# Performance work log

Measured on AMD Instinct MI355X. Metric: run time of the kernel, lower is better.

## Reference

```python
import jax, jax.numpy as jnp
import numpy as np

B, S, HID = 1, 2048, 4096
H, HKV, D = 32, 8, 128
ROT = 64  # partial_rotary_factor = 0.5
EPS = 1e-6
SCALE = D ** -0.5


def setup_inputs() -> dict:
    key = jax.random.key(0)
    ks = jax.random.split(key, 8)
    return {
        "hidden_states": jax.random.normal(ks[0], (B, S, HID), jnp.float32),
        "cos": jax.random.uniform(ks[1], (B, S, ROT), jnp.float32),
        "sin": jax.random.uniform(ks[2], (B, S, ROT), jnp.float32),
        "Wq": jax.random.normal(ks[3], (H * D, HID), jnp.float32) * 0.02,
        "Wk": jax.random.normal(ks[4], (HKV * D, HID), jnp.float32) * 0.02,
        "Wv": jax.random.normal(ks[5], (HKV * D, HID), jnp.float32) * 0.02,
        "Wo": jax.random.normal(ks[6], (H * D, HID), jnp.float32).T * 0.02,  # [HID, H*D]
        "q_norm_w": jnp.ones((D,), jnp.float32),
        "k_norm_w": jnp.ones((D,), jnp.float32),
    }


def _rmsnorm(x, w):
    var = jnp.mean(jnp.square(x), axis=-1, keepdims=True)
    return x * jax.lax.rsqrt(var + EPS) * w


def _rotate_half(x):
    x1, x2 = jnp.split(x, 2, axis=-1)
    return jnp.concatenate([-x2, x1], axis=-1)


def reference(hidden_states, cos, sin, Wq, Wk, Wv, Wo, q_norm_w, k_norm_w):
    b, s, _ = hidden_states.shape
    q = (hidden_states @ Wq.T).reshape(b, s, H, D)
    k = (hidden_states @ Wk.T).reshape(b, s, HKV, D)
    v = (hidden_states @ Wv.T).reshape(b, s, HKV, D)
    # per-head QK RMSNorm
    q = _rmsnorm(q, q_norm_w)
    k = _rmsnorm(k, k_norm_w)
    # partial RoPE on first ROT dims; cos/sin broadcast over head dim (unsqueeze_dim=2)
    cs = cos[:, :, None, :]  # [B,S,1,ROT]
    sn = sin[:, :, None, :]
    q_rot, q_pass = q[..., :ROT], q[..., ROT:]
    k_rot, k_pass = k[..., :ROT], k[..., ROT:]
    q_rot = q_rot * cs + _rotate_half(q_rot) * sn
    k_rot = k_rot * cs + _rotate_half(k_rot) * sn
    q = jnp.concatenate([q_rot, q_pass], axis=-1)
    k = jnp.concatenate([k_rot, k_pass], axis=-1)
    # GQA: expand kv heads to query heads
    rep = H // HKV
    k = jnp.repeat(k, rep, axis=2)  # [B,S,H,D]
    v = jnp.repeat(v, rep, axis=2)
    # causal SDPA, bsnd layout
    scores = jnp.einsum("bqhd,bkhd->bhqk", q, k) * SCALE
    causal = jnp.tril(jnp.ones((s, s), bool))
    scores = jnp.where(causal, scores, jnp.finfo(scores.dtype).min)
    attn = jax.nn.softmax(scores, axis=-1)
    out = jnp.einsum("bhqk,bkhd->bqhd", attn, v).reshape(b, s, H * D)
    return out @ Wo.T
```

## Files before the change

kernel.cpp:

```cpp
#include <hip/hip_runtime.h>
#include <hip/hip_bf16.h>

typedef __attribute__((ext_vector_type(8))) short bf16x8;
typedef __attribute__((ext_vector_type(4))) float f32x4;
typedef __hip_bfloat16 bf16;

#define S_LEN 2048
#define HIDDEN 4096
#define NH 32
#define NKV 8
#define DH 128
#define ROTD 64
#define QKVW 6144
#define KOFF 4096
#define VOFF 5120
#define ATT_SCALE 0.08838834764831845f
#define RMS_EPS 1e-6f
#define KPITCH 136
#define VPITCH 72

static __device__ __forceinline__ unsigned short f2bu(float f) {
    bf16 h = __float2bfloat16(f);
    return __builtin_bit_cast(unsigned short, h);
}

static __device__ __forceinline__ void load_lds_16(const bf16* g, bf16* l) {
    __builtin_amdgcn_global_load_lds((const __attribute__((address_space(1))) void*)g,
                                     (__attribute__((address_space(3))) void*)l, 16, 0, 0);
}

__global__ __launch_bounds__(256) void cast_f32_bf16(const float* __restrict__ src,
                                                     unsigned short* __restrict__ dst, int n4) {
    int i = blockIdx.x * 256 + threadIdx.x;
    if (i >= n4) return;
    float4 v = reinterpret_cast<const float4*>(src)[i];
    ushort4 o;
    o.x = f2bu(v.x); o.y = f2bu(v.y); o.z = f2bu(v.z); o.w = f2bu(v.w);
    reinterpret_cast<ushort4*>(dst)[i] = o;
}

template <typename OutT>
__global__ __launch_bounds__(256) void gemm_lds(const bf16* __restrict__ A,
                                                const bf16* __restrict__ B,
                                                OutT* __restrict__ C,
                                                int M, int N, int K) {
    __shared__ bf16 As[128 * 32];
    __shared__ bf16 Bs[128 * 32];
    const int tid  = threadIdx.x;
    const int lane = tid & 63;
    const int wave = tid >> 6;
    const int lq   = lane & 15;
    const int quad = lane >> 4;
    const int m0 = blockIdx.y * 128;
    const int n0 = blockIdx.x * 128;
    const int wm = (wave & 1) * 64;
    const int wn = (wave >> 1) * 64;

    f32x4 acc[4][4] = {};

    const int ar = tid >> 2;
    const int ac = (tid & 3) * 8;
    const bf16* Ag0 = A + (size_t)(m0 + ar) * K + ac;
    const bf16* Ag1 = Ag0 + (size_t)64 * K;
    const bf16* Bg0 = B + (size_t)(n0 + ar) * K + ac;
    const bf16* Bg1 = Bg0 + (size_t)64 * K;
    bf16* Asl0 = As + wave * 512;
    bf16* Asl1 = As + wave * 512 + 2048;
    bf16* Bsl0 = Bs + wave * 512;
    bf16* Bsl1 = Bs + wave * 512 + 2048;

    for (int k0 = 0; k0 < K; k0 += 32) {
        load_lds_16(Ag0 + k0, Asl0);
        load_lds_16(Ag1 + k0, Asl1);
        load_lds_16(Bg0 + k0, Bsl0);
        load_lds_16(Bg1 + k0, Bsl1);
        __syncthreads();
        bf16x8 av[4], bv[4];
#pragma unroll
        for (int i = 0; i < 4; ++i)
            av[i] = *reinterpret_cast<const bf16x8*>(As + (wm + i * 16 + lq) * 32 + quad * 8);
#pragma unroll
        for (int i = 0; i < 4; ++i)
            bv[i] = *reinterpret_cast<const bf16x8*>(Bs + (wn + i * 16 + lq) * 32 + quad * 8);
#pragma unroll
        for (int mt = 0; mt < 4; ++mt)
#pragma unroll
            for (int nt = 0; nt < 4; ++nt)
                acc[mt][nt] = __builtin_amdgcn_mfma_f32_16x16x32_bf16(av[mt], bv[nt], acc[mt][nt], 0, 0, 0);
        __syncthreads();
    }

#pragma unroll
    for (int mt = 0; mt < 4; ++mt)
#pragma unroll
        for (int nt = 0; nt < 4; ++nt)
#pragma unroll
            for (int r = 0; r < 4; ++r) {
                float v = acc[mt][nt][r];
                size_t idx = (size_t)(m0 + wm + mt * 16 + quad * 4 + r) * N + n0 + wn + nt * 16 + lq;
                if constexpr (sizeof(OutT) == 2) C[idx] = __float2bfloat16(v);
                else                             C[idx] = v;
            }
}

__global__ __launch_bounds__(256) void norm_rope(bf16* __restrict__ buf,
                                                 const float* __restrict__ w,
                                                 const float* __restrict__ cosp,
                                                 const float* __restrict__ sinp,
                                                 int log2nh, int stride, int coloff) {
    const int lane = threadIdx.x & 63;
    const int wave = threadIdx.x >> 6;
    const int row  = blockIdx.x * 4 + wave;
    const int s    = row >> log2nh;
    const int hh   = row & ((1 << log2nh) - 1);
    bf16* p = buf + (size_t)s * stride + coloff + hh * DH;

    float x1 = __bfloat162float(p[lane]);
    float x2 = __bfloat162float(p[64 + lane]);

    float ss = x1 * x1 + x2 * x2;
#pragma unroll
    for (int off = 1; off < 64; off <<= 1) ss += __shfl_xor(ss, off);
    float rs = rsqrtf(ss * (1.0f / 128.0f) + RMS_EPS);

    float y1 = x1 * rs * w[lane];
    float y2 = x2 * rs * w[64 + lane];

    float partner = __shfl_xor(y1, 32);
    float c  = cosp[(size_t)s * ROTD + lane];
    float sn = sinp[(size_t)s * ROTD + lane];
    float rot = (lane < 32) ? (y1 * c - partner * sn) : (y1 * c + partner * sn);

    p[lane]      = __float2bfloat16(rot);
    p[64 + lane] = __float2bfloat16(y2);
}

__global__ __launch_bounds__(256) void transpose_v(const bf16* __restrict__ v,
                                                   bf16* __restrict__ vt,
                                                   int stride, int colofs) {
    __shared__ bf16 t[32][65];
    const int c0 = blockIdx.x * 32;
    const int s0 = blockIdx.y * 64;
    {
        const int j  = threadIdx.x & 31;
        const int i0 = threadIdx.x >> 5;
#pragma unroll
        for (int p = 0; p < 8; ++p) {
            int si = p * 8 + i0;
            t[j][si] = v[(size_t)(s0 + si) * stride + colofs + c0 + j];
        }
    }
    __syncthreads();
    {
        const int ii = threadIdx.x & 63;
        const int j0 = threadIdx.x >> 6;
#pragma unroll
        for (int p = 0; p < 8; ++p) {
            int c = p * 4 + j0;
            vt[(size_t)(c0 + c) * S_LEN + s0 + ii] = t[c][ii];
        }
    }
}

struct FlashSmem {
    bf16 Ks[64][KPITCH];
    bf16 Vs[128][VPITCH];
    bf16 Ps[4][16][VPITCH];
};

static __device__ __forceinline__ void attn_qblock(int q0, int n_iter, int h, int kvh,
                                                   const bf16* __restrict__ QKV,
                                                   const bf16* __restrict__ VT,
                                                   bf16* __restrict__ O,
                                                   FlashSmem* sm) {
    const int tid  = threadIdx.x;
    const int lane = tid & 63;
    const int wave = tid >> 6;
    const int lq   = lane & 15;
    const int quad = lane >> 4;
    const int qr0  = q0 + wave * 16;

    bf16x8 qf[4];
    const bf16* qrow = QKV + (size_t)(qr0 + lq) * QKVW + h * DH + quad * 8;
#pragma unroll
    for (int i = 0; i < 4; ++i) {
        bf16x8 qv = *reinterpret_cast<const bf16x8*>(qrow + 32 * i);
#pragma unroll
        for (int j = 0; j < 8; ++j) {
            bf16 b = __builtin_bit_cast(bf16, (unsigned short)qv[j]);
            qv[j] = (short)__builtin_bit_cast(unsigned short,
                        __float2bfloat16(__bfloat162float(b) * ATT_SCALE));
        }
        qf[i] = qv;
    }

    f32x4 o[8];
#pragma unroll
    for (int t2 = 0; t2 < 8; ++t2) o[t2] = (f32x4){0.f, 0.f, 0.f, 0.f};
    float m_i[4], l_i[4];
#pragma unroll
    for (int r = 0; r < 4; ++r) { m_i[r] = -1e30f; l_i[r] = 0.f; }

    const bf16* kg = QKV + (size_t)(tid >> 2) * QKVW + KOFF + kvh * DH + (tid & 3) * 32;
    const bf16* vg = VT + (size_t)(kvh * DH + (tid >> 1)) * S_LEN + (tid & 1) * 32;
    bf16* ksl = &sm->Ks[tid >> 2][(tid & 3) * 32];
    bf16* vsl = &sm->Vs[tid >> 1][(tid & 1) * 32];
    bf16* pb  = &sm->Ps[wave][0][0];

    bf16x8 kreg[4], vreg[4];
#pragma unroll
    for (int c = 0; c < 4; ++c) {
        kreg[c] = *reinterpret_cast<const bf16x8*>(kg + 8 * c);
        vreg[c] = *reinterpret_cast<const bf16x8*>(vg + 8 * c);
    }

    for (int kt = 0; kt < n_iter; ++kt) {
        const int k0 = kt * 64;
#pragma unroll
        for (int c = 0; c < 4; ++c) {
            *reinterpret_cast<bf16x8*>(ksl + 8 * c) = kreg[c];
            *reinterpret_cast<bf16x8*>(vsl + 8 * c) = vreg[c];
        }
        __syncthreads();
        if (kt + 1 < n_iter) {
            const size_t kadv = (size_t)(kt + 1) * 64;
#pragma unroll
            for (int c = 0; c < 4; ++c) {
                kreg[c] = *reinterpret_cast<const bf16x8*>(kg + kadv * QKVW + 8 * c);
                vreg[c] = *reinterpret_cast<const bf16x8*>(vg + kadv + 8 * c);
            }
        }

        float p[4][4];
#pragma unroll
        for (int t = 0; t < 4; ++t) {
            f32x4 sacc = (f32x4){0.f, 0.f, 0.f, 0.f};
#pragma unroll
            for (int i = 0; i < 4; ++i) {
                bf16x8 kf = *reinterpret_cast<const bf16x8*>(&sm->Ks[t * 16 + lq][quad * 8 + 32 * i]);
                sacc = __builtin_amdgcn_mfma_f32_16x16x32_bf16(qf[i], kf, sacc, 0, 0, 0);
            }
#pragma unroll
            for (int r = 0; r < 4; ++r) {
                int qi = qr0 + quad * 4 + r;
                int ki = k0 + t * 16 + lq;
                p[t][r] = (ki > qi) ? -1e30f : sacc[r];
            }
        }

        float rowmax[4];
#pragma unroll
        for (int r = 0; r < 4; ++r)
            rowmax[r] = fmaxf(fmaxf(p[0][r], p[1][r]), fmaxf(p[2][r], p[3][r]));
#pragma unroll
        for (int off = 1; off < 16; off <<= 1)
#pragma unroll
            for (int r = 0; r < 4; ++r) rowmax[r] = fmaxf(rowmax[r], __shfl_xor(rowmax[r], off));

        float alpha[4];
#pragma unroll
        for (int r = 0; r < 4; ++r) {
            float mn = fmaxf(m_i[r], rowmax[r]);
            alpha[r] = __expf(m_i[r] - mn);
            m_i[r] = mn;
        }
#pragma unroll
        for (int t = 0; t < 4; ++t)
#pragma unroll
            for (int r = 0; r < 4; ++r) p[t][r] = __expf(p[t][r] - m_i[r]);

        float rsum[4];
#pragma unroll
        for (int r = 0; r < 4; ++r) rsum[r] = (p[0][r] + p[1][r]) + (p[2][r] + p[3][r]);
#pragma unroll
        for (int off = 1; off < 16; off <<= 1)
#pragma unroll
            for (int r = 0; r < 4; ++r) rsum[r] += __shfl_xor(rsum[r], off);
#pragma unroll
        for (int r = 0; r < 4; ++r) l_i[r] = l_i[r] * alpha[r] + rsum[r];

#pragma unroll
        for (int t = 0; t < 4; ++t)
#pragma unroll
            for (int r = 0; r < 4; ++r)
                pb[(quad * 4 + r) * VPITCH + t * 16 + lq] = __float2bfloat16(p[t][r]);
        __threadfence_block();

#pragma unroll
        for (int t2 = 0; t2 < 8; ++t2)
#pragma unroll
            for (int r = 0; r < 4; ++r) o[t2][r] *= alpha[r];

#pragma unroll
        for (int hh = 0; hh < 2; ++hh) {
            bf16x8 pa = *reinterpret_cast<const bf16x8*>(pb + lq * VPITCH + hh * 32 + quad * 8);
#pragma unroll
            for (int t2 = 0; t2 < 8; ++t2) {
                bf16x8 vf = *reinterpret_cast<const bf16x8*>(&sm->Vs[t2 * 16 + lq][hh * 32 + quad * 8]);
                o[t2] = __builtin_amdgcn_mfma_f32_16x16x32_bf16(pa, vf, o[t2], 0, 0, 0);
            }
        }
        __syncthreads();
    }

#pragma unroll
    for (int r = 0; r < 4; ++r) l_i[r] = 1.0f / l_i[r];
#pragma unroll
    for (int t2 = 0; t2 < 8; ++t2)
#pragma unroll
        for (int r = 0; r < 4; ++r)
            O[(size_t)(qr0 + quad * 4 + r) * (NH * DH) + h * DH + t2 * 16 + lq] =
                __float2bfloat16(o[t2][r] * l_i[r]);
}

__global__ __launch_bounds__(256) void flash_attn(const bf16* __restrict__ QKV,
                                                  const bf16* __restrict__ VT,
                                                  bf16* __restrict__ O) {
    __shared__ FlashSmem sm;
    const int b  = blockIdx.x;
    const int h  = b & 31;
    const int pr = b >> 5;
    const int kvh = h >> 2;
    attn_qblock((31 - pr) * 64, 32 - pr, h, kvh, QKV, VT, O, &sm);
    __syncthreads();
    attn_qblock(pr * 64,        pr + 1,  h, kvh, QKV, VT, O, &sm);
}

extern "C" void kernel_launch(void* const* d_in, const int* in_sizes, int n_in,
                              void* d_out, int out_size, void* d_ws, size_t ws_size,
                              hipStream_t stream) {
    const float* hs   = (const float*)d_in[0];
    const float* cosp = (const float*)d_in[1];
    const float* sinp = (const float*)d_in[2];
    const float* Wq   = (const float*)d_in[3];
    const float* Wk   = (const float*)d_in[4];
    const float* Wv   = (const float*)d_in[5];
    const float* Wo   = (const float*)d_in[6];
    const float* qw   = (const float*)d_in[7];
    const float* kw   = (const float*)d_in[8];
    float* out = (float*)d_out;

    char* ws = (char*)d_ws;
    size_t off = 0;
    auto carve = [&](size_t bytes) { char* p = ws + off; off += (bytes + 255) & ~(size_t)255; return p; };

    bf16* hsb  = (bf16*)carve((size_t)S_LEN * HIDDEN * 2);
    bf16* wqkv = (bf16*)carve((size_t)QKVW * HIDDEN * 2);
    bf16* wob  = (bf16*)carve((size_t)HIDDEN * NH * DH * 2);
    bf16* qkv  = (bf16*)carve((size_t)S_LEN * QKVW * 2);
    bf16* vtb  = (bf16*)carve((size_t)NKV * DH * S_LEN * 2);

    cast_f32_bf16<<<(S_LEN * HIDDEN / 4 + 255) / 256, 256, 0, stream>>>(hs, (unsigned short*)hsb, S_LEN * HIDDEN / 4);
    cast_f32_bf16<<<(NH * DH * HIDDEN / 4 + 255) / 256, 256, 0, stream>>>(Wq, (unsigned short*)wqkv, NH * DH * HIDDEN / 4);
    cast_f32_bf16<<<(NKV * DH * HIDDEN / 4 + 255) / 256, 256, 0, stream>>>(Wk, (unsigned short*)(wqkv + (size_t)KOFF * HIDDEN), NKV * DH * HIDDEN / 4);
    cast_f32_bf16<<<(NKV * DH * HIDDEN / 4 + 255) / 256, 256, 0, stream>>>(Wv, (unsigned short*)(wqkv + (size_t)VOFF * HIDDEN), NKV * DH * HIDDEN / 4);
    cast_f32_bf16<<<(HIDDEN * NH * DH / 4 + 255) / 256, 256, 0, stream>>>(Wo, (unsigned short*)wob, HIDDEN * NH * DH / 4);

    gemm_lds<bf16><<<dim3(QKVW / 128, S_LEN / 128), 256, 0, stream>>>(hsb, wqkv, qkv, S_LEN, QKVW, HIDDEN);

    norm_rope<<<S_LEN * NH / 4, 256, 0, stream>>>(qkv, qw, cosp, sinp, 5, QKVW, 0);
    norm_rope<<<S_LEN * NKV / 4, 256, 0, stream>>>(qkv, kw, cosp, sinp, 3, QKVW, KOFF);

    transpose_v<<<dim3(NKV * DH / 32, S_LEN / 64), 256, 0, stream>>>(qkv, vtb, QKVW, VOFF);

    bf16* aob = hsb;
    flash_attn<<<512, 256, 0, stream>>>(qkv, vtb, aob);

    gemm_lds<float><<<dim3(HIDDEN / 128, S_LEN / 128), 256, 0, stream>>>(aob, wob, out, S_LEN, HIDDEN, NH * DH);
}
```

Measured before the change: 567.8 us.

## Replace GEMM with 256x256-tile double-buffered pipelined swizzled LDS kernel

Replaces the simple 128x128 single-buffered GEMM used for the QKV and output projections with a 512-thread kernel that computes 256x256 tiles and uses K-steps of 64. Global-to-LDS loads are double-buffered and issued in quarter-tile stages interleaved with MFMA phases, using explicit waitcnt, barriers and setprio. LDS addresses get an XOR swizzle to avoid bank conflicts, and workgroup IDs are remapped to improve L2 locality. The goal is better data reuse and overlap of memory with compute. The cost is heavy LDS use (128KB per block), fragile hand-written synchronisation, and fewer workgroups: 192 and 128 blocks on 256 CUs.

```diff
diff --git a/kernel.cpp b/kernel.cpp
--- a/kernel.cpp
+++ b/kernel.cpp
@@ -19,6 +19,10 @@
 #define KPITCH 136
 #define VPITCH 72
 
+#define BAR() __builtin_amdgcn_s_barrier()
+#define VMCNT(n) asm volatile("s_waitcnt vmcnt(" #n ")" ::: "memory")
+#define LGKM(n)  asm volatile("s_waitcnt lgkmcnt(" #n ")" ::: "memory")
+
 static __device__ __forceinline__ unsigned short f2bu(float f) {
     bf16 h = __float2bfloat16(f);
     return __builtin_bit_cast(unsigned short, h);
@@ -39,68 +43,149 @@
     reinterpret_cast<ushort4*>(dst)[i] = o;
 }
 
+#define LDA_SUB(bufi, half) do {                                                        \
+    const bf16* _ab = &As[bufi][half][0];                                               \
+    _Pragma("unroll") for (int mf = 0; mf < 4; ++mf) {                                  \
+        const int _r = arow + mf * 16;                                                  \
+        _Pragma("unroll") for (int kk = 0; kk < 2; ++kk)                                \
+            av[mf][kk] = *reinterpret_cast<const bf16x8*>(                              \
+                _ab + (((_r << 6) + kk * 32 + quad * 8) ^ xorv));                       \
+    } } while (0)
+
+#define LDB_SUB(bufi, half, set) do {                                                   \
+    const bf16* _bb = &Bs[bufi][half][0];                                               \
+    _Pragma("unroll") for (int nf = 0; nf < 2; ++nf) {                                  \
+        const int _r = brow + nf * 16;                                                  \
+        _Pragma("unroll") for (int kk = 0; kk < 2; ++kk)                                \
+            bv[set][nf][kk] = *reinterpret_cast<const bf16x8*>(                         \
+                _bb + (((_r << 6) + kk * 32 + quad * 8) ^ xorv));                       \
+    } } while (0)
+
+#define MMQ(mh, nh, set) do {                                                           \
+    _Pragma("unroll") for (int mf = 0; mf < 4; ++mf)                                    \
+    _Pragma("unroll") for (int nf = 0; nf < 2; ++nf)                                    \
+    _Pragma("unroll") for (int kk = 0; kk < 2; ++kk)                                    \
+        acc[mh][nh][mf][nf] = __builtin_amdgcn_mfma_f32_16x16x32_bf16(                  \
+            av[mf][kk], bv[set][nf][kk], acc[mh][nh][mf][nf], 0, 0, 0);                 \
+    } while (0)
+
+#define STAGE_A(bufi, half, tau) do {                                                   \
+    const bf16* _s = Abase + (size_t)(half) * 128 * K + (size_t)(tau) * 64;             \
+    load_lds_16(_s + sro0, &As[bufi][half][e0]);                                        \
+    load_lds_16(_s + sro1, &As[bufi][half][e1]); } while (0)
+
+#define STAGE_B(bufi, half, tau) do {                                                   \
+    const bf16* _s = Bbase + (size_t)(half) * 128 * K + (size_t)(tau) * 64;             \
+    load_lds_16(_s + sro0, &Bs[bufi][half][e0]);                                        \
+    load_lds_16(_s + sro1, &Bs[bufi][half][e1]); } while (0)
+
 template <typename OutT>
-__global__ __launch_bounds__(256) void gemm_lds(const bf16* __restrict__ A,
-                                                const bf16* __restrict__ B,
-                                                OutT* __restrict__ C,
-                                                int M, int N, int K) {
-    __shared__ bf16 As[128 * 32];
-    __shared__ bf16 Bs[128 * 32];
+__global__ __launch_bounds__(512, 2) void gemm256(const bf16* __restrict__ A,
+                                                  const bf16* __restrict__ B,
+                                                  OutT* __restrict__ C,
+                                                  int M, int N, int K) {
+    __shared__ bf16 As[2][2][128 * 64];
+    __shared__ bf16 Bs[2][2][128 * 64];
+
     const int tid  = threadIdx.x;
     const int lane = tid & 63;
-    const int wave = tid >> 6;
     const int lq   = lane & 15;
     const int quad = lane >> 4;
-    const int m0 = blockIdx.y * 128;
-    const int n0 = blockIdx.x * 128;
-    const int wm = (wave & 1) * 64;
-    const int wn = (wave >> 1) * 64;
-
-    f32x4 acc[4][4] = {};
-
-    const int ar = tid >> 2;
-    const int ac = (tid & 3) * 8;
-    const bf16* Ag0 = A + (size_t)(m0 + ar) * K + ac;
-    const bf16* Ag1 = Ag0 + (size_t)64 * K;
-    const bf16* Bg0 = B + (size_t)(n0 + ar) * K + ac;
-    const bf16* Bg1 = Bg0 + (size_t)64 * K;
-    bf16* Asl0 = As + wave * 512;
-    bf16* Asl1 = As + wave * 512 + 2048;
-    bf16* Bsl0 = Bs + wave * 512;
-    bf16* Bsl1 = Bs + wave * 512 + 2048;
-
-    for (int k0 = 0; k0 < K; k0 += 32) {
-        load_lds_16(Ag0 + k0, Asl0);
-        load_lds_16(Ag1 + k0, Asl1);
-        load_lds_16(Bg0 + k0, Bsl0);
-        load_lds_16(Bg1 + k0, Bsl1);
-        __syncthreads();
-        bf16x8 av[4], bv[4];
-#pragma unroll
-        for (int i = 0; i < 4; ++i)
-            av[i] = *reinterpret_cast<const bf16x8*>(As + (wm + i * 16 + lq) * 32 + quad * 8);
-#pragma unroll
-        for (int i = 0; i < 4; ++i)
-            bv[i] = *reinterpret_cast<const bf16x8*>(Bs + (wn + i * 16 + lq) * 32 + quad * 8);
-#pragma unroll
-        for (int mt = 0; mt < 4; ++mt)
-#pragma unroll
-            for (int nt = 0; nt < 4; ++nt)
-                acc[mt][nt] = __builtin_amdgcn_mfma_f32_16x16x32_bf16(av[mt], bv[nt], acc[mt][nt], 0, 0, 0);
-        __syncthreads();
-    }
-
-#pragma unroll
-    for (int mt = 0; mt < 4; ++mt)
-#pragma unroll
-        for (int nt = 0; nt < 4; ++nt)
-#pragma unroll
-            for (int r = 0; r < 4; ++r) {
-                float v = acc[mt][nt][r];
-                size_t idx = (size_t)(m0 + wm + mt * 16 + quad * 4 + r) * N + n0 + wn + nt * 16 + lq;
-                if constexpr (sizeof(OutT) == 2) C[idx] = __float2bfloat16(v);
-                else                             C[idx] = v;
-            }
+    const int wave = tid >> 6;
+    const int wr   = wave >> 2;
+    const int wc   = wave & 3;
+
+    const int nwg = gridDim.x;
+    const int cpx = nwg >> 3;
+    const int wg  = (blockIdx.x & 7) * cpx + (blockIdx.x >> 3);
+    const int ntn = N >> 8;
+    const int m0  = (wg / ntn) << 8;
+    const int n0  = (wg % ntn) << 8;
+
+    const int NT = K >> 6;
+
+    const int d0 = tid * 16;
+    const int d1 = 8192 + tid * 16;
+    const int o0 = d0 ^ (((d0 >> 7) & 7) << 4);
+    const int o1 = d1 ^ (((d1 >> 7) & 7) << 4);
+    const int e0 = d0 >> 1;
+    const int e1 = d1 >> 1;
+    const size_t sro0 = (size_t)((o0 >> 1) >> 6) * K + ((o0 >> 1) & 63);
+    const size_t sro1 = (size_t)((o1 >> 1) >> 6) * K + ((o1 >> 1) & 63);
+    const bf16* Abase = A + (size_t)m0 * K;
+    const bf16* Bbase = B + (size_t)n0 * K;
+
+    const int arow = wr * 64 + lq;
+    const int brow = wc * 32 + lq;
+    const int xorv = (lq & 7) << 3;
+
+    f32x4  acc[2][2][4][2] = {};
+    bf16x8 av[4][2];
+    bf16x8 bv[2][2][2];
+
+    STAGE_B(0, 0, 0); STAGE_A(0, 0, 0); STAGE_B(0, 1, 0); STAGE_A(0, 1, 0);
+    STAGE_B(1, 0, 1); STAGE_A(1, 0, 1); STAGE_B(1, 1, 1);
+    VMCNT(6);
+    BAR();
+
+    for (int t = 0; t < NT; ++t) {
+        const int buf = t & 1;
+
+        LDA_SUB(buf, 0);
+        LDB_SUB(buf, 0, 0);
+        if (t + 1 < NT) STAGE_A(buf ^ 1, 1, t + 1);
+        LGKM(8);
+        BAR();
+        LGKM(0);
+        __builtin_amdgcn_s_setprio(1);
+        MMQ(0, 0, 0);
+        __builtin_amdgcn_s_setprio(0);
+        BAR();
+
+        LDB_SUB(buf, 1, 1);
+        if (t + 2 < NT) STAGE_B(buf, 0, t + 2);
+        BAR();
+        LGKM(0);
+        __builtin_amdgcn_s_setprio(1);
+        MMQ(0, 1, 1);
+        __builtin_amdgcn_s_setprio(0);
+        BAR();
+
+        LDA_SUB(buf, 1);
+        if (t + 2 < NT) STAGE_A(buf, 0, t + 2);
+        BAR();
+        LGKM(0);
+        __builtin_amdgcn_s_setprio(1);
+        MMQ(1, 1, 1);
+        __builtin_amdgcn_s_setprio(0);
+        BAR();
+
+        if (t + 2 < NT) STAGE_B(buf, 1, t + 2);
+        BAR();
+        __builtin_amdgcn_s_setprio(1);
+        MMQ(1, 0, 0);
+        __builtin_amdgcn_s_setprio(0);
+        if (t < NT - 2) { VMCNT(6); } else { VMCNT(0); }
+        BAR();
+    }
+
+#pragma unroll
+    for (int mh = 0; mh < 2; ++mh)
+#pragma unroll
+        for (int nh = 0; nh < 2; ++nh)
+#pragma unroll
+            for (int mf = 0; mf < 4; ++mf)
+#pragma unroll
+                for (int nf = 0; nf < 2; ++nf)
+#pragma unroll
+                    for (int r = 0; r < 4; ++r) {
+                        const int row = m0 + mh * 128 + wr * 64 + mf * 16 + quad * 4 + r;
+                        const int col = n0 + nh * 128 + wc * 32 + nf * 16 + lq;
+                        const float v = acc[mh][nh][mf][nf][r];
+                        const size_t idx = (size_t)row * N + col;
+                        if constexpr (sizeof(OutT) == 2) C[idx] = __float2bfloat16(v);
+                        else                             C[idx] = v;
+                    }
 }
 
 __global__ __launch_bounds__(256) void norm_rope(bf16* __restrict__ buf,
@@ -356,7 +441,7 @@
     cast_f32_bf16<<<(NKV * DH * HIDDEN / 4 + 255) / 256, 256, 0, stream>>>(Wv, (unsigned short*)(wqkv + (size_t)VOFF * HIDDEN), NKV * DH * HIDDEN / 4);
     cast_f32_bf16<<<(HIDDEN * NH * DH / 4 + 255) / 256, 256, 0, stream>>>(Wo, (unsigned short*)wob, HIDDEN * NH * DH / 4);
 
-    gemm_lds<bf16><<<dim3(QKVW / 128, S_LEN / 128), 256, 0, stream>>>(hsb, wqkv, qkv, S_LEN, QKVW, HIDDEN);
+    gemm256<bf16><<<dim3((S_LEN / 256) * (QKVW / 256)), 512, 0, stream>>>(hsb, wqkv, qkv, S_LEN, QKVW, HIDDEN);
 
     norm_rope<<<S_LEN * NH / 4, 256, 0, stream>>>(qkv, qw, cosp, sinp, 5, QKVW, 0);
     norm_rope<<<S_LEN * NKV / 4, 256, 0, stream>>>(qkv, kw, cosp, sinp, 3, QKVW, KOFF);
@@ -366,5 +451,5 @@
     bf16* aob = hsb;
     flash_attn<<<512, 256, 0, stream>>>(qkv, vtb, aob);
 
-    gemm_lds<float><<<dim3(HIDDEN / 128, S_LEN / 128), 256, 0, stream>>>(aob, wob, out, S_LEN, HIDDEN, NH * DH);
-}
+    gemm256<float><<<dim3((S_LEN / 256) * (HIDDEN / 256)), 512, 0, stream>>>(aob, wob, out, S_LEN, HIDDEN, NH * DH);
+}
```

Measured after the change: 563.0 us. Within noise of the previous version (-0.8%).
